# Performance work log

Hardware: AMD Instinct MI355X
Metric: run time of the kernel (lower is better)

Reference implementation:

```python
import jax, jax.numpy as jnp
import numpy as np

HIDDEN = 4096
NUM_HEADS = 32
HEAD_DIM = HIDDEN // NUM_HEADS  # 128


def apply_rope(x, cos, sin):
    # x: (B, H, S, D); cos/sin: (S, D//2)
    d2 = x.shape[-1] // 2
    x1, x2 = x[..., :d2], x[..., d2:]
    c = cos[None, None, :x.shape[2], :]
    s = sin[None, None, :x.shape[2], :]
    return jnp.concatenate([x1 * c - x2 * s, x2 * c + x1 * s], axis=-1)


def setup_inputs() -> dict:
    key = jax.random.key(0)
    ks = jax.random.split(key, 7)
    B, S = 2, 2048
    scale = 1.0 / np.sqrt(HIDDEN)
    return {
        "x": jax.random.normal(ks[0], (B, S, HIDDEN), dtype=jnp.float32),
        "cos": jax.random.normal(ks[1], (S, HEAD_DIM // 2), dtype=jnp.float32),
        "sin": jax.random.normal(ks[2], (S, HEAD_DIM // 2), dtype=jnp.float32),
        "wq": jax.random.normal(ks[3], (HIDDEN, HIDDEN), dtype=jnp.float32) * scale,
        "wk": jax.random.normal(ks[4], (HIDDEN, HIDDEN), dtype=jnp.float32) * scale,
        "wv": jax.random.normal(ks[5], (HIDDEN, HIDDEN), dtype=jnp.float32) * scale,
        "wo": jax.random.normal(ks[6], (HIDDEN, HIDDEN), dtype=jnp.float32) * scale,
    }


def reference(x, cos, sin, wq, wk, wv, wo):
    B, S, _ = x.shape
    # nn.Linear(x) = x @ W.T  (weights stored (out, in))
    def proj(w):
        t = jnp.einsum('bsd,ed->bse', x, w)
        return t.reshape(B, S, NUM_HEADS, HEAD_DIM).transpose(0, 2, 1, 3)
    q, k, v = proj(wq), proj(wk), proj(wv)
    q = apply_rope(q, cos, sin)
    k = apply_rope(k, cos, sin)
    scale = HEAD_DIM ** (-0.5)
    attn = jnp.einsum('bhqd,bhkd->bhqk', q, k) * scale  # (B,H,S,S)
    causal = jnp.tril(jnp.ones((S, S), dtype=bool))
    attn = jnp.where(causal[None, None], attn, -jnp.inf)
    attn = jax.nn.softmax(attn, axis=-1)
    out = jnp.einsum('bhqk,bhkd->bhqd', attn, v)
    out = out.transpose(0, 2, 1, 3).reshape(B, S, HIDDEN)
    return jnp.einsum('bsd,ed->bse', out, wo)
```

## Files before the change

### kernel.cpp

```cpp
#include <hip/hip_runtime.h>
#include <stdint.h>

#define DEV __device__ __forceinline__

typedef __attribute__((ext_vector_type(8))) short short8v;
typedef __attribute__((ext_vector_type(4))) short short4v;
typedef __attribute__((ext_vector_type(4))) float f32x4;
typedef __attribute__((ext_vector_type(16))) float f32x16;

DEV uint16_t f2bf(float f) {
  union { float f; uint32_t u; } x; x.f = f;
  return (uint16_t)((x.u + 0x7FFFu + ((x.u >> 16) & 1u)) >> 16);
}
DEV float bf2f(uint16_t v) {
  union { uint32_t u; float f; } x; x.u = ((uint32_t)v) << 16;
  return x.f;
}

DEV void gload_lds16(const uint16_t* g, uint16_t* l) {
  __builtin_amdgcn_global_load_lds(
      (const __attribute__((address_space(1))) uint32_t*)g,
      (__attribute__((address_space(3))) uint32_t*)l, 16, 0, 0);
}

__global__ void convert5_kernel(const float* __restrict__ x,
                                const float* __restrict__ wq,
                                const float* __restrict__ wk,
                                const float* __restrict__ wv,
                                const float* __restrict__ wo,
                                uint16_t* __restrict__ xb, uint16_t* __restrict__ wqb,
                                uint16_t* __restrict__ wkb, uint16_t* __restrict__ wvb,
                                uint16_t* __restrict__ wob, int n4) {
  const int which = blockIdx.y;
  const float* in = which == 0 ? x : which == 1 ? wq : which == 2 ? wk
                                   : which == 3 ? wv : wo;
  uint16_t* out = which == 0 ? xb : which == 1 ? wqb : which == 2 ? wkb
                                  : which == 3 ? wvb : wob;
  int i = blockIdx.x * blockDim.x + threadIdx.x;
  if (i >= n4) return;
  float4 v = reinterpret_cast<const float4*>(in)[i];
  short4v o;
  o[0] = (short)f2bf(v.x); o[1] = (short)f2bf(v.y);
  o[2] = (short)f2bf(v.z); o[3] = (short)f2bf(v.w);
  *reinterpret_cast<short4v*>(out + (size_t)i * 4) = o;
}

template <int F32OUT>
__global__ __launch_bounds__(512, 2) void gemm256_kernel(
    const uint16_t* __restrict__ A, const uint16_t* __restrict__ Bt,
    float* __restrict__ Cf, uint16_t* __restrict__ Cb, int M, int N, int K) {
  __shared__ uint16_t smem[65536];
  uint16_t* As0 = smem;
  uint16_t* As1 = smem + 16384;
  uint16_t* Bs0 = smem + 32768;
  uint16_t* Bs1 = smem + 49152;

  const int tid = threadIdx.x;
  const int lane = tid & 63, w = tid >> 6;
  const int ln16 = lane & 15, g = lane >> 4;
  const int wr = w >> 2, wc = w & 3;

  const int nbx = gridDim.x;
  int bid = blockIdx.y * nbx + blockIdx.x;
  int nb = nbx * gridDim.y;
  int cpx = nb >> 3;
  int sw = (bid & 7) * cpx + (bid >> 3);
  const int m0 = (sw / nbx) * 256, n0 = (sw % nbx) * 256;

  const int trow = tid >> 3;
  const int tcol = ((tid & 7) ^ (trow & 7)) * 8;
  const uint16_t* srcA = A + (size_t)(m0 + trow) * K + tcol;
  const int brow = (w >> 2) * 64 + (w & 3) * 8 + (lane >> 3);
  const int bcol = ((lane & 7) ^ ((lane >> 3) & 7)) * 8;
  const uint16_t* srcB = Bt + (size_t)(n0 + brow) * K + bcol;
  const int dstAw = w * 512;
  const int dstBw = ((w >> 2) * 64 + (w & 3) * 8) * 64;

#define STA(buf, q, kt) \
  gload_lds16(srcA + (size_t)((q) * 64) * K + (kt) * 64, (buf) + (q) * 4096 + dstAw)
#define STB(buf, nq, c, kt) \
  gload_lds16(srcB + (size_t)((c) * 128 + (nq) * 32) * K + (kt) * 64, \
              (buf) + ((c) * 128 + (nq) * 32) * 64 + dstBw)
#define LDA(buf, mq, mi, ks) \
  (*reinterpret_cast<const short8v*>( \
      (buf) + (wr * 128 + (mq) * 64 + (mi) * 16 + ln16) * 64 + \
      ((((ks) * 4 + g) ^ (ln16 & 7)) * 8)))
#define LDB(buf, nq, ni, ks) \
  (*reinterpret_cast<const short8v*>( \
      (buf) + (wc * 64 + (nq) * 32 + (ni) * 16 + ln16) * 64 + \
      ((((ks) * 4 + g) ^ (ln16 & 7)) * 8)))

  f32x4 acc[8][4];
#pragma unroll
  for (int i = 0; i < 8; ++i)
#pragma unroll
    for (int j = 0; j < 4; ++j) acc[i][j] = f32x4{0.f, 0.f, 0.f, 0.f};

  STA(As0, 0, 0); STA(As0, 2, 0); STA(As0, 1, 0); STA(As0, 3, 0);
  STB(Bs0, 0, 0, 0); STB(Bs0, 0, 1, 0); STB(Bs0, 1, 0, 0); STB(Bs0, 1, 1, 0);
  STA(As1, 0, 1); STA(As1, 2, 1);
  STB(Bs1, 0, 0, 1); STB(Bs1, 0, 1, 1); STB(Bs1, 1, 0, 1); STB(Bs1, 1, 1, 1);
  asm volatile("s_waitcnt vmcnt(6)" ::: "memory");
  __builtin_amdgcn_sched_barrier(0);
  __builtin_amdgcn_s_barrier();

  uint16_t *Ac = As0, *An = As1, *Bc = Bs0, *Bn = Bs1;
  short8v af[4][2], bf0[2][2], bf1[2][2];

  const int NT = K >> 6;
  for (int t = 0; t < NT; ++t) {
    const int k1 = (t + 1 < NT) ? t + 1 : NT - 1;
    const int k2 = (t + 2 < NT) ? t + 2 : NT - 1;
#pragma unroll
    for (int mi = 0; mi < 4; ++mi) { af[mi][0] = LDA(Ac, 0, mi, 0); af[mi][1] = LDA(Ac, 0, mi, 1); }
#pragma unroll
    for (int ni = 0; ni < 2; ++ni) { bf0[ni][0] = LDB(Bc, 0, ni, 0); bf0[ni][1] = LDB(Bc, 0, ni, 1); }
    STA(An, 1, k1); STA(An, 3, k1);
    __builtin_amdgcn_s_barrier();
    asm volatile("s_waitcnt lgkmcnt(0)" ::: "memory");
    __builtin_amdgcn_sched_barrier(0);
    __builtin_amdgcn_s_setprio(1);
#pragma unroll
    for (int ks = 0; ks < 2; ++ks)
#pragma unroll
      for (int mi = 0; mi < 4; ++mi)
#pragma unroll
        for (int ni = 0; ni < 2; ++ni)
          acc[mi][ni] = __builtin_amdgcn_mfma_f32_16x16x32_bf16(af[mi][ks], bf0[ni][ks], acc[mi][ni], 0, 0, 0);
    __builtin_amdgcn_s_setprio(0);
    __builtin_amdgcn_s_barrier();
#pragma unroll
    for (int ni = 0; ni < 2; ++ni) { bf1[ni][0] = LDB(Bc, 1, ni, 0); bf1[ni][1] = LDB(Bc, 1, ni, 1); }
    STA(Ac, 0, k2); STA(Ac, 2, k2);
    __builtin_amdgcn_s_barrier();
    asm volatile("s_waitcnt lgkmcnt(0)" ::: "memory");
    __builtin_amdgcn_sched_barrier(0);
    __builtin_amdgcn_s_setprio(1);
#pragma unroll
    for (int ks = 0; ks < 2; ++ks)
#pragma unroll
      for (int mi = 0; mi < 4; ++mi)
#pragma unroll
        for (int ni = 0; ni < 2; ++ni)
          acc[mi][2 + ni] = __builtin_amdgcn_mfma_f32_16x16x32_bf16(af[mi][ks], bf1[ni][ks], acc[mi][2 + ni], 0, 0, 0);
    __builtin_amdgcn_s_setprio(0);
    __builtin_amdgcn_s_barrier();
#pragma unroll
    for (int mi = 0; mi < 4; ++mi) { af[mi][0] = LDA(Ac, 1, mi, 0); af[mi][1] = LDA(Ac, 1, mi, 1); }
    STB(Bc, 0, 0, k2); STB(Bc, 0, 1, k2);
    __builtin_amdgcn_s_barrier();
    asm volatile("s_waitcnt lgkmcnt(0)" ::: "memory");
    __builtin_amdgcn_sched_barrier(0);
    __builtin_amdgcn_s_setprio(1);
#pragma unroll
    for (int ks = 0; ks < 2; ++ks)
#pragma unroll
      for (int mi = 0; mi < 4; ++mi)
#pragma unroll
        for (int ni = 0; ni < 2; ++ni)
          acc[4 + mi][2 + ni] = __builtin_amdgcn_mfma_f32_16x16x32_bf16(af[mi][ks], bf1[ni][ks], acc[4 + mi][2 + ni], 0, 0, 0);
    __builtin_amdgcn_s_setprio(0);
    __builtin_amdgcn_s_barrier();
    STB(Bc, 1, 0, k2); STB(Bc, 1, 1, k2);
    __builtin_amdgcn_s_barrier();
    __builtin_amdgcn_s_setprio(1);
#pragma unroll
    for (int ks = 0; ks < 2; ++ks)
#pragma unroll
      for (int mi = 0; mi < 4; ++mi)
#pragma unroll
        for (int ni = 0; ni < 2; ++ni)
          acc[4 + mi][ni] = __builtin_amdgcn_mfma_f32_16x16x32_bf16(af[mi][ks], bf0[ni][ks], acc[4 + mi][ni], 0, 0, 0);
    __builtin_amdgcn_s_setprio(0);
    asm volatile("s_waitcnt vmcnt(6)" ::: "memory");
    __builtin_amdgcn_sched_barrier(0);
    __builtin_amdgcn_s_barrier();
    uint16_t* tp = Ac; Ac = An; An = tp;
    tp = Bc; Bc = Bn; Bn = tp;
  }

#pragma unroll
  for (int gmi = 0; gmi < 8; ++gmi)
#pragma unroll
    for (int r = 0; r < 4; ++r) {
      int row = m0 + wr * 128 + gmi * 16 + g * 4 + r;
#pragma unroll
      for (int gni = 0; gni < 4; ++gni) {
        int col = n0 + wc * 64 + gni * 16 + ln16;
        if (F32OUT)
          Cf[(size_t)row * N + col] = acc[gmi][gni][r];
        else
          Cb[(size_t)row * N + col] = (uint16_t)f2bf(acc[gmi][gni][r]);
      }
    }
#undef STA
#undef STB
#undef LDA
#undef LDB
}

__global__ void rope_kernel(uint16_t* __restrict__ buf,
                            const float* __restrict__ cost,
                            const float* __restrict__ sint) {
  int idx = blockIdx.x * blockDim.x + threadIdx.x;
  int j8 = idx & 7;
  int h = (idx >> 3) & 31;
  int s = (idx >> 8) & 2047;
  int b = idx >> 19;
  size_t base = ((size_t)(b * 2048 + s)) * 4096 + h * 128 + j8 * 8;
  short8v x1 = *reinterpret_cast<const short8v*>(buf + base);
  short8v x2 = *reinterpret_cast<const short8v*>(buf + base + 64);
  float4 c0 = *reinterpret_cast<const float4*>(cost + s * 64 + j8 * 8);
  float4 c1 = *reinterpret_cast<const float4*>(cost + s * 64 + j8 * 8 + 4);
  float4 s0 = *reinterpret_cast<const float4*>(sint + s * 64 + j8 * 8);
  float4 s1 = *reinterpret_cast<const float4*>(sint + s * 64 + j8 * 8 + 4);
  float c[8] = {c0.x, c0.y, c0.z, c0.w, c1.x, c1.y, c1.z, c1.w};
  float sn[8] = {s0.x, s0.y, s0.z, s0.w, s1.x, s1.y, s1.z, s1.w};
  short8v o1, o2;
#pragma unroll
  for (int e = 0; e < 8; ++e) {
    float a = bf2f((uint16_t)x1[e]);
    float bb = bf2f((uint16_t)x2[e]);
    o1[e] = (short)f2bf(a * c[e] - bb * sn[e]);
    o2[e] = (short)f2bf(bb * c[e] + a * sn[e]);
  }
  *reinterpret_cast<short8v*>(buf + base) = o1;
  *reinterpret_cast<short8v*>(buf + base + 64) = o2;
}

__global__ __launch_bounds__(256, 2) void flash_kernel(
    const uint16_t* __restrict__ Q, const uint16_t* __restrict__ K,
    const uint16_t* __restrict__ V, uint16_t* __restrict__ O) {
  constexpr int S = 2048, HID = 4096;
  __shared__ uint16_t Ks[64 * 128];
  __shared__ uint16_t Vt[128 * 64];

  const int tid = threadIdx.x;
  const int lane = tid & 63, w = tid >> 6;
  const int l31 = lane & 31, hi = lane >> 5;
  const int bh = blockIdx.y;
  const int b = bh >> 5, h = bh & 31;
  const int bt = 15 - blockIdx.x;
  const int q0 = bt * 128;
  const int q0w = q0 + w * 32;
  const size_t base = (size_t)b * S * HID + (size_t)h * 128;
  const int swz = (l31 & 7) << 3;

  const int ksr = tid >> 4;
  const int ksc = (tid & 15) * 8;
  const int vk4 = tid & 15;
  const int vdc = tid >> 4;

  short8v qf[8];
  {
    const uint16_t* qrow = Q + base + (size_t)(q0w + l31) * HID + hi * 8;
#pragma unroll
    for (int c = 0; c < 8; ++c)
      qf[c] = *reinterpret_cast<const short8v*>(qrow + c * 16);
  }

  f32x16 o[4];
#pragma unroll
  for (int db = 0; db < 4; ++db)
#pragma unroll
    for (int r = 0; r < 16; ++r) o[db][r] = 0.f;
  float m_run = -1e30f, l_run = 0.f;
  const float cl2e = 0.12751025f;

  short8v kp[4], vp[4];

#pragma unroll
  for (int i = 0; i < 4; ++i)
    kp[i] = *reinterpret_cast<const short8v*>(
        K + base + (size_t)(i * 16 + ksr) * HID + ksc);
#pragma unroll
  for (int j = 0; j < 4; ++j)
    vp[j] = *reinterpret_cast<const short8v*>(
        V + base + (size_t)(4 * vk4 + j) * HID + vdc * 8);
#pragma unroll
  for (int i = 0; i < 4; ++i) {
    int row = i * 16 + ksr;
    *reinterpret_cast<short8v*>(Ks + row * 128 + (ksc ^ ((row & 7) << 3))) = kp[i];
  }
#pragma unroll
  for (int e = 0; e < 8; ++e) {
    int row = vdc * 8 + e;
    short4v pk; pk[0] = vp[0][e]; pk[1] = vp[1][e]; pk[2] = vp[2][e]; pk[3] = vp[3][e];
    *reinterpret_cast<short4v*>(Vt + row * 64 + ((vk4 * 4) ^ ((row & 7) << 3))) = pk;
  }
  __syncthreads();

  const int ntiles = bt * 2 + 2;
  for (int kt = 0; kt < ntiles; ++kt) {
    const int kb = kt * 64;
    const bool havenext = (kt + 1 < ntiles);
    if (havenext) {
      const int kb2 = kb + 64;
#pragma unroll
      for (int i = 0; i < 4; ++i)
        kp[i] = *reinterpret_cast<const short8v*>(
            K + base + (size_t)(kb2 + i * 16 + ksr) * HID + ksc);
#pragma unroll
      for (int j = 0; j < 4; ++j)
        vp[j] = *reinterpret_cast<const short8v*>(
            V + base + (size_t)(kb2 + 4 * vk4 + j) * HID + vdc * 8);
    }

    if (kb <= q0w + 31) {
      f32x16 s0, s1;
#pragma unroll
      for (int r = 0; r < 16; ++r) { s0[r] = 0.f; s1[r] = 0.f; }
      __builtin_amdgcn_s_setprio(1);
#pragma unroll
      for (int c = 0; c < 8; ++c) {
        int col = c * 16 + hi * 8;
        short8v kf0 = *reinterpret_cast<const short8v*>(Ks + l31 * 128 + (col ^ swz));
        short8v kf1 = *reinterpret_cast<const short8v*>(Ks + (32 + l31) * 128 + (col ^ swz));
        s0 = __builtin_amdgcn_mfma_f32_32x32x16_bf16(kf0, qf[c], s0, 0, 0, 0);
        s1 = __builtin_amdgcn_mfma_f32_32x32x16_bf16(kf1, qf[c], s1, 0, 0, 0);
      }
      __builtin_amdgcn_s_setprio(0);
#pragma unroll
      for (int r = 0; r < 16; ++r) { s0[r] *= cl2e; s1[r] *= cl2e; }
      if (kb + 63 > q0w) {
        const int qg = q0w + l31;
#pragma unroll
        for (int r = 0; r < 16; ++r) {
          int kl = (r & 3) + 8 * (r >> 2) + 4 * hi;
          if (kb + kl > qg) s0[r] = -1e30f;
          if (kb + 32 + kl > qg) s1[r] = -1e30f;
        }
      }
      float mx = s0[0];
#pragma unroll
      for (int r = 1; r < 16; ++r) mx = fmaxf(mx, s0[r]);
#pragma unroll
      for (int r = 0; r < 16; ++r) mx = fmaxf(mx, s1[r]);
      mx = fmaxf(mx, __shfl_xor(mx, 32));
      if (__any(mx > m_run + 8.0f)) {
        float nm = fmaxf(m_run, mx);
        float f = __builtin_amdgcn_exp2f(m_run - nm);
        l_run *= f;
#pragma unroll
        for (int db = 0; db < 4; ++db)
#pragma unroll
          for (int r = 0; r < 16; ++r) o[db][r] *= f;
        m_run = nm;
      }
      float rs = 0.f;
#pragma unroll
      for (int r = 0; r < 16; ++r) { s0[r] = __builtin_amdgcn_exp2f(s0[r] - m_run); rs += s0[r]; }
#pragma unroll
      for (int r = 0; r < 16; ++r) { s1[r] = __builtin_amdgcn_exp2f(s1[r] - m_run); rs += s1[r]; }
      rs += __shfl_xor(rs, 32);
      l_run += rs;
      uint32_t c0[8], c1[8];
#pragma unroll
      for (int i = 0; i < 4; ++i) {
        asm("v_cvt_pk_bf16_f32 %0, %1, %2" : "=v"(c0[i])     : "v"(s0[4 * i]),     "v"(s0[4 * i + 1]));
        asm("v_cvt_pk_bf16_f32 %0, %1, %2" : "=v"(c1[i])     : "v"(s0[4 * i + 2]), "v"(s0[4 * i + 3]));
        asm("v_cvt_pk_bf16_f32 %0, %1, %2" : "=v"(c0[4 + i]) : "v"(s1[4 * i]),     "v"(s1[4 * i + 1]));
        asm("v_cvt_pk_bf16_f32 %0, %1, %2" : "=v"(c1[4 + i]) : "v"(s1[4 * i + 2]), "v"(s1[4 * i + 3]));
      }
      short8v pa[4];
#pragma unroll
      for (int t = 0; t < 4; ++t) {
        int st = t >> 1, ts = t & 1;
        uint32_t a0 = c0[st * 4 + 2 * ts],     a1 = c1[st * 4 + 2 * ts];
        uint32_t b0 = c0[st * 4 + 2 * ts + 1], b1 = c1[st * 4 + 2 * ts + 1];
        uint32_t sb0 = (uint32_t)__shfl_xor((int)b0, 32);
        uint32_t sb1 = (uint32_t)__shfl_xor((int)b1, 32);
        uint32_t sa0 = (uint32_t)__shfl_xor((int)a0, 32);
        uint32_t sa1 = (uint32_t)__shfl_xor((int)a1, 32);
        union { uint32_t u[4]; short8v v; } pk;
        pk.u[0] = hi ? sb0 : a0;
        pk.u[1] = hi ? sb1 : a1;
        pk.u[2] = hi ? b0 : sa0;
        pk.u[3] = hi ? b1 : sa1;
        pa[t] = pk.v;
      }
      __builtin_amdgcn_s_setprio(1);
#pragma unroll
      for (int t = 0; t < 4; ++t) {
        int col = t * 16 + hi * 8;
#pragma unroll
        for (int db = 0; db < 4; ++db) {
          short8v vf = *reinterpret_cast<const short8v*>(
              Vt + (db * 32 + l31) * 64 + (col ^ swz));
          o[db] = __builtin_amdgcn_mfma_f32_32x32x16_bf16(vf, pa[t], o[db], 0, 0, 0);
        }
      }
      __builtin_amdgcn_s_setprio(0);
    }
    __syncthreads();
    if (havenext) {
#pragma unroll
      for (int i = 0; i < 4; ++i) {
        int row = i * 16 + ksr;
        *reinterpret_cast<short8v*>(Ks + row * 128 + (ksc ^ ((row & 7) << 3))) = kp[i];
      }
#pragma unroll
      for (int e = 0; e < 8; ++e) {
        int row = vdc * 8 + e;
        short4v pk; pk[0] = vp[0][e]; pk[1] = vp[1][e]; pk[2] = vp[2][e]; pk[3] = vp[3][e];
        *reinterpret_cast<short4v*>(Vt + row * 64 + ((vk4 * 4) ^ ((row & 7) << 3))) = pk;
      }
      __syncthreads();
    }
  }

  float inv = 1.f / l_run;
  uint16_t* orow = O + base + (size_t)(q0w + l31) * HID;
#pragma unroll
  for (int db = 0; db < 4; ++db)
#pragma unroll
    for (int rq = 0; rq < 4; ++rq) {
      short4v st4;
#pragma unroll
      for (int e = 0; e < 4; ++e) st4[e] = (short)f2bf(o[db][rq * 4 + e] * inv);
      *reinterpret_cast<short4v*>(orow + db * 32 + rq * 8 + hi * 4) = st4;
    }
}

extern "C" void kernel_launch(void* const* d_in, const int* in_sizes, int n_in,
                              void* d_out, int out_size, void* d_ws, size_t ws_size,
                              hipStream_t stream) {
  const float* x    = (const float*)d_in[0];
  const float* cosb = (const float*)d_in[1];
  const float* sinb = (const float*)d_in[2];
  const float* wq   = (const float*)d_in[3];
  const float* wk   = (const float*)d_in[4];
  const float* wv   = (const float*)d_in[5];
  const float* wo   = (const float*)d_in[6];
  float* out = (float*)d_out;

  const size_t BUF = 33554432;
  if (ws_size < 8 * BUF) return;
  char* ws = (char*)d_ws;
  uint16_t* xb  = (uint16_t*)(ws + 0 * BUF);
  uint16_t* wqb = (uint16_t*)(ws + 1 * BUF);
  uint16_t* wkb = (uint16_t*)(ws + 2 * BUF);
  uint16_t* wvb = (uint16_t*)(ws + 3 * BUF);
  uint16_t* wob = (uint16_t*)(ws + 4 * BUF);
  uint16_t* qb  = (uint16_t*)(ws + 5 * BUF);
  uint16_t* kb  = (uint16_t*)(ws + 6 * BUF);
  uint16_t* vb  = (uint16_t*)(ws + 7 * BUF);
  uint16_t* ab  = xb;

  const int nElem = 2 * 2048 * 4096;
  dim3 cgrid(nElem / 4 / 256, 5);
  convert5_kernel<<<cgrid, 256, 0, stream>>>(x, wq, wk, wv, wo,
                                             xb, wqb, wkb, wvb, wob, nElem / 4);

  dim3 ggrid(16, 16), gblk(512);
  gemm256_kernel<0><<<ggrid, gblk, 0, stream>>>(xb, wqb, nullptr, qb, 4096, 4096, 4096);
  gemm256_kernel<0><<<ggrid, gblk, 0, stream>>>(xb, wkb, nullptr, kb, 4096, 4096, 4096);
  gemm256_kernel<0><<<ggrid, gblk, 0, stream>>>(xb, wvb, nullptr, vb, 4096, 4096, 4096);

  dim3 rgrid(1048576 / 256);
  rope_kernel<<<rgrid, 256, 0, stream>>>(qb, cosb, sinb);
  rope_kernel<<<rgrid, 256, 0, stream>>>(kb, cosb, sinb);

  dim3 fgrid(16, 64);
  flash_kernel<<<fgrid, 256, 0, stream>>>(qb, kb, vb, ab);

  gemm256_kernel<1><<<ggrid, gblk, 0, stream>>>(ab, wob, out, nullptr, 4096, 4096, 4096);
}
```

Before: 713.8 us.

## Double-buffer K/V in LDS and load K directly via global_load_lds

Doubles the K and V shared-memory tiles so the next tile is written into the alternate buffer while the current one is consumed, which removes one of the two barriers per iteration. K is now staged with direct global-to-LDS loads that apply the XOR swizzle through the source address, so it no longer passes through registers. This frees registers and overlaps the K fetch with compute. LDS use doubles to 64KB per block, which may limit occupancy at two blocks per CU. Correctness also relies on the async LDS writes having completed before the single barrier.

```diff
diff --git a/kernel.cpp b/kernel.cpp
--- a/kernel.cpp
+++ b/kernel.cpp
@@ -232,8 +232,8 @@
     const uint16_t* __restrict__ Q, const uint16_t* __restrict__ K,
     const uint16_t* __restrict__ V, uint16_t* __restrict__ O) {
   constexpr int S = 2048, HID = 4096;
-  __shared__ uint16_t Ks[64 * 128];
-  __shared__ uint16_t Vt[128 * 64];
+  __shared__ uint16_t Ks[2][64 * 128];
+  __shared__ uint16_t Vt[2][128 * 64];
 
   const int tid = threadIdx.x;
   const int lane = tid & 63, w = tid >> 6;
@@ -246,10 +246,21 @@
   const size_t base = (size_t)b * S * HID + (size_t)h * 128;
   const int swz = (l31 & 7) << 3;
 
-  const int ksr = tid >> 4;
-  const int ksc = (tid & 15) * 8;
+  const int kr_g = lane >> 4;
+  const int kre = w * 16 + kr_g;
+  const int kro = w * 16 + 4 + kr_g;
+  const uint16_t* kse = K + base + (size_t)kre * HID + (((lane & 15) ^ (kr_g & 7)) * 8);
+  const uint16_t* kso = K + base + (size_t)kro * HID + (((lane & 15) ^ ((4 + kr_g) & 7)) * 8);
   const int vk4 = tid & 15;
   const int vdc = tid >> 4;
+
+#define STAGEK(dst, kb0)                                                     \
+  do {                                                                       \
+    gload_lds16(kse + (size_t)(kb0) * HID,       (dst) + (w * 16 + 0) * 128);  \
+    gload_lds16(kso + (size_t)(kb0) * HID,       (dst) + (w * 16 + 4) * 128);  \
+    gload_lds16(kse + (size_t)((kb0) + 8) * HID, (dst) + (w * 16 + 8) * 128);  \
+    gload_lds16(kso + (size_t)((kb0) + 8) * HID, (dst) + (w * 16 + 12) * 128); \
+  } while (0)
 
   short8v qf[8];
   {
@@ -267,26 +278,18 @@
   float m_run = -1e30f, l_run = 0.f;
   const float cl2e = 0.12751025f;
 
-  short8v kp[4], vp[4];
-
-#pragma unroll
-  for (int i = 0; i < 4; ++i)
-    kp[i] = *reinterpret_cast<const short8v*>(
-        K + base + (size_t)(i * 16 + ksr) * HID + ksc);
+  short8v vp[4];
+
+  STAGEK(&Ks[0][0], 0);
 #pragma unroll
   for (int j = 0; j < 4; ++j)
     vp[j] = *reinterpret_cast<const short8v*>(
         V + base + (size_t)(4 * vk4 + j) * HID + vdc * 8);
 #pragma unroll
-  for (int i = 0; i < 4; ++i) {
-    int row = i * 16 + ksr;
-    *reinterpret_cast<short8v*>(Ks + row * 128 + (ksc ^ ((row & 7) << 3))) = kp[i];
-  }
-#pragma unroll
   for (int e = 0; e < 8; ++e) {
     int row = vdc * 8 + e;
     short4v pk; pk[0] = vp[0][e]; pk[1] = vp[1][e]; pk[2] = vp[2][e]; pk[3] = vp[3][e];
-    *reinterpret_cast<short4v*>(Vt + row * 64 + ((vk4 * 4) ^ ((row & 7) << 3))) = pk;
+    *reinterpret_cast<short4v*>(&Vt[0][0] + row * 64 + ((vk4 * 4) ^ ((row & 7) << 3))) = pk;
   }
   __syncthreads();
 
@@ -294,16 +297,16 @@
   for (int kt = 0; kt < ntiles; ++kt) {
     const int kb = kt * 64;
     const bool havenext = (kt + 1 < ntiles);
+    uint16_t* ksc = &Ks[kt & 1][0];
+    uint16_t* vtc = &Vt[kt & 1][0];
+    uint16_t* ksn = &Ks[(kt + 1) & 1][0];
+    uint16_t* vtn = &Vt[(kt + 1) & 1][0];
     if (havenext) {
-      const int kb2 = kb + 64;
-#pragma unroll
-      for (int i = 0; i < 4; ++i)
-        kp[i] = *reinterpret_cast<const short8v*>(
-            K + base + (size_t)(kb2 + i * 16 + ksr) * HID + ksc);
+      STAGEK(ksn, kb + 64);
 #pragma unroll
       for (int j = 0; j < 4; ++j)
         vp[j] = *reinterpret_cast<const short8v*>(
-            V + base + (size_t)(kb2 + 4 * vk4 + j) * HID + vdc * 8);
+            V + base + (size_t)(kb + 64 + 4 * vk4 + j) * HID + vdc * 8);
     }
 
     if (kb <= q0w + 31) {
@@ -314,8 +317,8 @@
 #pragma unroll
       for (int c = 0; c < 8; ++c) {
         int col = c * 16 + hi * 8;
-        short8v kf0 = *reinterpret_cast<const short8v*>(Ks + l31 * 128 + (col ^ swz));
-        short8v kf1 = *reinterpret_cast<const short8v*>(Ks + (32 + l31) * 128 + (col ^ swz));
+        short8v kf0 = *reinterpret_cast<const short8v*>(ksc + l31 * 128 + (col ^ swz));
+        short8v kf1 = *reinterpret_cast<const short8v*>(ksc + (32 + l31) * 128 + (col ^ swz));
         s0 = __builtin_amdgcn_mfma_f32_32x32x16_bf16(kf0, qf[c], s0, 0, 0, 0);
         s1 = __builtin_amdgcn_mfma_f32_32x32x16_bf16(kf1, qf[c], s1, 0, 0, 0);
       }
@@ -386,27 +389,21 @@
 #pragma unroll
         for (int db = 0; db < 4; ++db) {
           short8v vf = *reinterpret_cast<const short8v*>(
-              Vt + (db * 32 + l31) * 64 + (col ^ swz));
+              vtc + (db * 32 + l31) * 64 + (col ^ swz));
           o[db] = __builtin_amdgcn_mfma_f32_32x32x16_bf16(vf, pa[t], o[db], 0, 0, 0);
         }
       }
       __builtin_amdgcn_s_setprio(0);
     }
-    __syncthreads();
     if (havenext) {
-#pragma unroll
-      for (int i = 0; i < 4; ++i) {
-        int row = i * 16 + ksr;
-        *reinterpret_cast<short8v*>(Ks + row * 128 + (ksc ^ ((row & 7) << 3))) = kp[i];
-      }
 #pragma unroll
       for (int e = 0; e < 8; ++e) {
         int row = vdc * 8 + e;
         short4v pk; pk[0] = vp[0][e]; pk[1] = vp[1][e]; pk[2] = vp[2][e]; pk[3] = vp[3][e];
-        *reinterpret_cast<short4v*>(Vt + row * 64 + ((vk4 * 4) ^ ((row & 7) << 3))) = pk;
-      }
-      __syncthreads();
+        *reinterpret_cast<short4v*>(vtn + row * 64 + ((vk4 * 4) ^ ((row & 7) << 3))) = pk;
+      }
     }
+    __syncthreads();
   }
 
   float inv = 1.f / l_run;
@@ -420,6 +417,7 @@
       for (int e = 0; e < 4; ++e) st4[e] = (short)f2bf(o[db][rq * 4 + e] * inv);
       *reinterpret_cast<short4v*>(orow + db * 32 + rq * 8 + hi * 4) = st4;
     }
+#undef STAGEK
 }
 
 extern "C" void kernel_launch(void* const* d_in, const int* in_sizes, int n_in,
```

New measurement: 721.8 us. No clear change (+1.1%).
